# Kernel tuning notes

Hardware: AMD Instinct MI355X
Metric: run time of the kernel (lower is better)

The kernel has to match this reference:

```python
import jax, jax.numpy as jnp
import numpy as np

DIM, NHEADS = 1536, 12
HEAD_DIM = DIM // NHEADS  # 128

def _rope_params(max_pos, d):
    inv = 1.0 / (10000.0 ** (np.arange(0, d, 2, dtype=np.float64) / d))
    ang = np.outer(np.arange(max_pos, dtype=np.float64), inv)
    return np.stack([np.cos(ang), np.sin(ang)], -1).astype(np.float32)  # [max_pos, d//2, 2]

def setup_inputs() -> dict:
    key = jax.random.key(0)
    ks = jax.random.split(key, 8)
    B, F, H, W = 1, 3, 30, 52
    L = F * H * W  # 4680
    def w(k):
        return jax.random.normal(k, (DIM, DIM), jnp.float32) * 0.02
    # Wan rope table: head_dim=128 -> segments of real dim 44, 42, 42 (complex 22,21,21)
    freqs = np.concatenate([_rope_params(1024, 44), _rope_params(1024, 42), _rope_params(1024, 42)], axis=1)
    return {
        "x": jax.random.normal(ks[0], (B, L, DIM), jnp.float32),
        "wq": w(ks[1]), "bq": jnp.zeros((DIM,), jnp.float32),
        "wk": w(ks[2]), "bk": jnp.zeros((DIM,), jnp.float32),
        "wv": w(ks[3]), "bv": jnp.zeros((DIM,), jnp.float32),
        "wo": w(ks[4]), "bo": jnp.zeros((DIM,), jnp.float32),
        "gq": jnp.ones((DIM,), jnp.float32),
        "gk": jnp.ones((DIM,), jnp.float32),
        "freqs": jnp.asarray(freqs),                       # [1024, 64, 2] (cos, sin)
        "seq_lens": jnp.array([L], jnp.int64),
        "grid_sizes": jnp.array([[F, H, W]], jnp.int64),
        "F": F, "H": H, "W": W,
        "sink_size": 1, "local_attn_size": 2,
    }

def _rmsnorm(x, g, eps=1e-6):
    xf = x.astype(jnp.float32)
    return xf * jax.lax.rsqrt(jnp.mean(xf * xf, -1, keepdims=True) + eps) * g

def _rope_table(freqs, F, H, W):
    # freqs: [1024, 64, 2]; split complex dims [22, 21, 21] for (t, h, w)
    c = freqs.shape[1]
    s0 = c - 2 * (c // 3)          # 22
    s1 = c // 3                    # 21
    ft = jnp.broadcast_to(freqs[:F, :s0].reshape(F, 1, 1, s0, 2), (F, H, W, s0, 2))
    fh = jnp.broadcast_to(freqs[:H, s0:s0 + s1].reshape(1, H, 1, s1, 2), (F, H, W, s1, 2))
    fw = jnp.broadcast_to(freqs[:W, s0 + s1:].reshape(1, 1, W, s1, 2), (F, H, W, s1, 2))
    return jnp.concatenate([ft, fh, fw], -2).reshape(F * H * W, c, 2)  # [L, c, 2]

def _apply_rope(t, fr):
    # t: [B, L, n, d]; fr: [L, c, 2] with c = d // 2; complex multiply in real arithmetic
    B, L, n, d = t.shape
    c = d // 2
    tr = t.reshape(B, L, n, c, 2)
    a, b = tr[..., 0], tr[..., 1]
    cos = fr[None, :, None, :, 0]
    sin = fr[None, :, None, :, 1]
    out = jnp.stack([a * cos - b * sin, a * sin + b * cos], -1)
    return out.reshape(B, L, n, d)

def reference(x, wq, bq, wk, bk, wv, bv, wo, bo, gq, gk, freqs, seq_lens, grid_sizes,
              F, H, W, sink_size, local_attn_size):
    B, L, dim = x.shape
    n, d = NHEADS, HEAD_DIM
    q = _rmsnorm(x @ wq.T + bq, gq).reshape(B, L, n, d)
    k = _rmsnorm(x @ wk.T + bk, gk).reshape(B, L, n, d)
    v = (x @ wv.T + bv).reshape(B, L, n, d)
    fr = _rope_table(freqs, F, H, W)
    rq = _apply_rope(q, fr)
    rk = _apply_rope(k, fr)
    # sink + causal local-window block mask at frame granularity
    frame = jnp.arange(L) // (H * W)
    fq, fk = frame[:, None], frame[None, :]
    allow = (fk <= fq) & ((fk < sink_size) | (fq - fk < local_attn_size))  # [L, L]
    scores = jnp.einsum('blnd,bmnd->bnlm', rq, rk) / jnp.sqrt(jnp.float32(d))
    scores = jnp.where(allow[None, None], scores, -jnp.inf)
    p = jax.nn.softmax(scores, axis=-1)
    out = jnp.einsum('bnlm,bmnd->blnd', p, v).reshape(B, L, dim)
    return out @ wo.T + bo
```

## Files before the change

### kernel.cpp

```cpp
#include <hip/hip_runtime.h>

#define L_SEQ 4680
#define DIMSZ 1536
#define NHEAD 12
#define HDIM 128
#define FRAME 1560
#define NKT_ALL 74
#define SCALE_L2E 0.12751743f
#define WSZ 2359296
#define XSZ 7274496
#define PMPITCH 4736

typedef float f32x4 __attribute__((ext_vector_type(4)));
typedef _Float16 f16;
typedef _Float16 f16x2 __attribute__((ext_vector_type(2)));
typedef _Float16 f16x4 __attribute__((ext_vector_type(4)));
typedef _Float16 f16x8 __attribute__((ext_vector_type(8)));
typedef unsigned short u16;

__device__ __forceinline__ void gll16(const void* g, void* l) {
  __builtin_amdgcn_global_load_lds(
      (const __attribute__((address_space(1))) unsigned int*)g,
      (__attribute__((address_space(3))) unsigned int*)l, 16, 0, 0);
}

__global__ __launch_bounds__(256) void split_a16(
    const float* __restrict__ A, int R, f16* __restrict__ out) {
  const int rt = blockIdx.x, kt = blockIdx.y;
  const int t = threadIdx.x;
  const int row = t >> 1, c0 = (t & 1) * 16;
  const int gr = min(rt * 128 + row, R - 1);
  const float* src = &A[(size_t)gr * DIMSZ + kt * 32 + c0];
  float f[16];
#pragma unroll
  for (int i = 0; i < 4; ++i) *(float4*)&f[i * 4] = *(const float4*)&src[i * 4];
  size_t obase = ((size_t)(rt * 48 + kt)) * 4096 + row * 32;
#pragma unroll
  for (int cc = 0; cc < 2; ++cc) {
    f16x8 o;
#pragma unroll
    for (int i = 0; i < 8; ++i) o[i] = (f16)f[cc * 8 + i];
    int s = (c0 >> 3) + cc;
    *(f16x8*)&out[obase + ((s * 8) ^ ((row & 3) * 8))] = o;
  }
}

__global__ __launch_bounds__(256) void split_w16x3(
    const float* __restrict__ s0, const float* __restrict__ s1, const float* __restrict__ s2,
    f16* __restrict__ hi_base, f16* __restrict__ lo_base) {
  const int z = blockIdx.z;
  const float* A = z == 0 ? s0 : (z == 1 ? s1 : s2);
  f16* hi = hi_base + (size_t)z * WSZ;
  f16* lo8 = lo_base + (size_t)z * WSZ;
  const int rt = blockIdx.x, kt = blockIdx.y;
  const int t = threadIdx.x;
  const int row = t >> 1, c0 = (t & 1) * 16;
  const float* src = &A[(size_t)(rt * 128 + row) * DIMSZ + kt * 32 + c0];
  float f[16];
#pragma unroll
  for (int i = 0; i < 4; ++i) *(float4*)&f[i * 4] = *(const float4*)&src[i * 4];
  size_t obase = ((size_t)(rt * 48 + kt)) * 4096 + row * 32;
#pragma unroll
  for (int cc = 0; cc < 2; ++cc) {
    f16x8 oh, ol;
#pragma unroll
    for (int i = 0; i < 8; ++i) {
      float v = f[cc * 8 + i];
      f16 h = (f16)v;
      oh[i] = h;
      ol[i] = (f16)((v - (float)h) * 256.0f);
    }
    int s = (c0 >> 3) + cc;
    size_t off = obase + ((s * 8) ^ ((row & 3) * 8));
    *(f16x8*)&hi[off] = oh;
    *(f16x8*)&lo8[off] = ol;
  }
}

__global__ __launch_bounds__(256) void split_w16(
    const float* __restrict__ A, f16* __restrict__ hi, f16* __restrict__ lo8) {
  const int rt = blockIdx.x, kt = blockIdx.y;
  const int t = threadIdx.x;
  const int row = t >> 1, c0 = (t & 1) * 16;
  const float* src = &A[(size_t)(rt * 128 + row) * DIMSZ + kt * 32 + c0];
  float f[16];
#pragma unroll
  for (int i = 0; i < 4; ++i) *(float4*)&f[i * 4] = *(const float4*)&src[i * 4];
  size_t obase = ((size_t)(rt * 48 + kt)) * 4096 + row * 32;
#pragma unroll
  for (int cc = 0; cc < 2; ++cc) {
    f16x8 oh, ol;
#pragma unroll
    for (int i = 0; i < 8; ++i) {
      float v = f[cc * 8 + i];
      f16 h = (f16)v;
      oh[i] = h;
      ol[i] = (f16)((v - (float)h) * 256.0f);
    }
    int s = (c0 >> 3) + cc;
    size_t off = obase + ((s * 8) ^ ((row & 3) * 8));
    *(f16x8*)&hi[off] = oh;
    *(f16x8*)&lo8[off] = ol;
  }
}

__global__ __launch_bounds__(256, 3) void gemm_f16(
    const f16* __restrict__ A, const f16* __restrict__ Wh, const f16* __restrict__ Wl,
    const float* __restrict__ b0, const float* __restrict__ b1, const float* __restrict__ b2,
    float* __restrict__ C, int M) {
  __shared__ f16 S[2][3][4096];
  const int t = threadIdx.x;
  const int lane = t & 63, w = t >> 6;
  const int g = lane >> 4, ln = lane & 15;
  const int wm = w >> 1, wn = w & 1;
  const int mt = blockIdx.x, nt = blockIdx.y;
  const int which = nt / 12, ntw = nt - which * 12;
  const float* bias = which == 0 ? b0 : (which == 1 ? b1 : b2);
  const f16* srcs[3] = {A + (size_t)mt * 48 * 4096,
                        Wh + ((size_t)which * 12 + ntw) * 48 * 4096,
                        Wl + ((size_t)which * 12 + ntw) * 48 * 4096};
  float* Cw = C + (size_t)which * ((size_t)L_SEQ * DIMSZ);
  f32x4 acc[4][4] = {};
#pragma unroll
  for (int a = 0; a < 3; ++a)
#pragma unroll
    for (int i = 0; i < 2; ++i)
      gll16(srcs[a] + (i * 256 + t) * 8, &S[0][a][(i * 256 + t) * 8]);
  int buf = 0;
  const f16 sc = (f16)0.00390625f;
  for (int kt = 0; kt < 48; ++kt) {
    __syncthreads();
    if (kt + 1 < 48) {
      int b = buf ^ 1;
#pragma unroll
      for (int a = 0; a < 3; ++a)
#pragma unroll
        for (int i = 0; i < 2; ++i)
          gll16(srcs[a] + (size_t)(kt + 1) * 4096 + (i * 256 + t) * 8,
                &S[b][a][(i * 256 + t) * 8]);
    }
    f16x8 af[4], as[4], wh4[4], wl4[4];
#pragma unroll
    for (int mi = 0; mi < 4; ++mi) {
      int row = wm * 64 + mi * 16 + ln;
      int off = row * 32 + ((g * 8) ^ ((row & 3) * 8));
      af[mi] = *(const f16x8*)&S[buf][0][off];
#pragma unroll
      for (int i = 0; i < 8; ++i) as[mi][i] = af[mi][i] * sc;
    }
#pragma unroll
    for (int ni = 0; ni < 4; ++ni) {
      int row = wn * 64 + ni * 16 + ln;
      int off = row * 32 + ((g * 8) ^ ((row & 3) * 8));
      wh4[ni] = *(const f16x8*)&S[buf][1][off];
      wl4[ni] = *(const f16x8*)&S[buf][2][off];
    }
#pragma unroll
    for (int mi = 0; mi < 4; ++mi)
#pragma unroll
      for (int ni = 0; ni < 4; ++ni) {
        acc[mi][ni] = __builtin_amdgcn_mfma_f32_16x16x32_f16(af[mi], wh4[ni], acc[mi][ni], 0, 0, 0);
        acc[mi][ni] = __builtin_amdgcn_mfma_f32_16x16x32_f16(as[mi], wl4[ni], acc[mi][ni], 0, 0, 0);
      }
    buf ^= 1;
  }
#pragma unroll
  for (int mi = 0; mi < 4; ++mi)
#pragma unroll
    for (int ni = 0; ni < 4; ++ni) {
      int col = ntw * 128 + wn * 64 + ni * 16 + ln;
      float bv = bias[col];
#pragma unroll
      for (int r = 0; r < 4; ++r) {
        int row = mt * 128 + wm * 64 + mi * 16 + 4 * g + r;
        if (row < M) Cw[(size_t)row * DIMSZ + col] = acc[mi][ni][r] + bv;
      }
    }
}

__global__ __launch_bounds__(256) void norm_rope(
    const float* __restrict__ qf, const float* __restrict__ kf,
    const float* __restrict__ gq, const float* __restrict__ gk,
    const float* __restrict__ freqs, f16* __restrict__ q16, f16* __restrict__ k16) {
  const int pos = blockIdx.x;
  const bool isq = blockIdx.y == 0;
  const float* row = (isq ? qf : kf) + (size_t)pos * DIMSZ;
  const float* g = isq ? gq : gk;
  const int t = threadIdx.x;
  float2 ab[3];
  float ss = 0.f;
#pragma unroll
  for (int i = 0; i < 3; ++i) {
    ab[i] = *(const float2*)&row[2 * (t + 256 * i)];
    ss += ab[i].x * ab[i].x + ab[i].y * ab[i].y;
  }
#pragma unroll
  for (int m = 32; m; m >>= 1) ss += __shfl_xor(ss, m);
  __shared__ float part[4];
  if ((t & 63) == 0) part[t >> 6] = ss;
  __syncthreads();
  const float tot = part[0] + part[1] + part[2] + part[3];
  float scale = rsqrtf(tot * (1.f / DIMSZ) + 1e-6f);
  if (isq) scale *= SCALE_L2E;
  const int f = pos / FRAME;
  const int rem = pos - f * FRAME;
  const int hh = rem / 52;
  const int ww = rem - hh * 52;
  const int kt = pos >> 6, kk = pos & 63;
#pragma unroll
  for (int i = 0; i < 3; ++i) {
    const int p = t + 256 * i;
    const int c = p & 63;
    const int h = p >> 6;
    const int pr = c < 22 ? f : (c < 43 ? hh : ww);
    const float cs = freqs[(pr * 64 + c) * 2 + 0];
    const float sn = freqs[(pr * 64 + c) * 2 + 1];
    const float a = ab[i].x * scale * g[2 * p];
    const float b = ab[i].y * scale * g[2 * p + 1];
    f16x2 o;
    o[0] = (f16)(a * cs - b * sn);
    o[1] = (f16)(a * sn + b * cs);
    if (isq) {
      *(f16x2*)&q16[(size_t)pos * DIMSZ + 2 * p] = o;
    } else {
      const int s = c >> 2;
      size_t base = ((size_t)(h * NKT_ALL + kt)) << 13;
      *(f16x2*)&k16[base + kk * 128 + ((s * 8) ^ ((kk & 7) * 8)) + (c & 3) * 2] = o;
    }
  }
}

__global__ __launch_bounds__(256) void vconvert(const float* __restrict__ v, f16* __restrict__ v16) {
  __shared__ f16 Ls[64][136];
  const int kt = blockIdx.x, h = blockIdx.y, t = threadIdx.x;
#pragma unroll
  for (int p = 0; p < 8; ++p) {
    int e = p * 1024 + t * 4;
    int kk = e >> 7, d = e & 127;
    int gr = kt * 64 + kk;
    float4 val = make_float4(0.f, 0.f, 0.f, 0.f);
    if (gr < L_SEQ) val = *(const float4*)&v[(size_t)gr * DIMSZ + h * HDIM + d];
    f16x4 o;
    o[0] = (f16)val.x; o[1] = (f16)val.y; o[2] = (f16)val.z; o[3] = (f16)val.w;
    *(f16x4*)&Ls[kk][d] = o;
  }
  __syncthreads();
  f16* out = v16 + (((size_t)(h * NKT_ALL + kt)) << 13);
#pragma unroll
  for (int p = 0; p < 4; ++p) {
    int idx = p * 256 + t;
    int d = idx >> 3, c = idx & 7;
    const int nbb = (c & 1) * 2;
    const int g4 = (c >> 1) * 4;
    f16x8 o;
#pragma unroll
    for (int i = 0; i < 8; ++i) o[i] = Ls[(nbb + (i >> 2)) * 16 + g4 + (i & 3)][d];
    *(f16x8*)&out[d * 64 + 8 * (c ^ (d & 7))] = o;
  }
}

__global__ __launch_bounds__(256, 2) void attn_split(
    const f16* __restrict__ q16, const f16* __restrict__ k16,
    const f16* __restrict__ v16, float* __restrict__ pO,
    float* __restrict__ pm, float* __restrict__ pl) {
  __shared__ f16 Ks[2][8192];
  __shared__ f16 Vt[8192];
  __shared__ float Os[4][16][20];
  const int b = blockIdx.x;
  const int qt = 36 - b / 24;
  const int rem = b % 24;
  const int s = rem / 12;
  const int h = rem % 12;
  const int q0 = qt * 128;
  const int t = threadIdx.x;
  const int lane = t & 63, w = t >> 6;
  const int g = lane >> 4, ln = lane & 15;

  f16x8 qa[2][4];
  int klim[2];
  float m_run[2], l_run[2];
#pragma unroll
  for (int mi = 0; mi < 2; ++mi) {
    int qrow = min(q0 + w * 32 + mi * 16 + ln, L_SEQ - 1);
    klim[mi] = (qrow / FRAME + 1) * FRAME;
    m_run[mi] = -1e30f;
    l_run[mi] = 0.f;
    const f16* qb = &q16[(size_t)qrow * DIMSZ + h * HDIM + g * 8];
#pragma unroll
    for (int kc = 0; kc < 4; ++kc) qa[mi][kc] = *(const f16x8*)&qb[kc * 32];
  }
  const int klim0 = __shfl(klim[0], 0);
  f32x4 acc[2][8] = {};

  const int rmax = min(q0 + 127, L_SEQ - 1);
  const int nkt = ((rmax / FRAME + 1) * FRAME + 63) >> 6;
  const size_t hbase = ((size_t)h * NKT_ALL) << 13;

  f16x8 vv0, vv1, vv2, vv3;
  {
    const f16* tv = v16 + hbase + ((size_t)s << 13) + t * 8;
    vv0 = *(const f16x8*)(tv);
    vv1 = *(const f16x8*)(tv + 2048);
    vv2 = *(const f16x8*)(tv + 4096);
    vv3 = *(const f16x8*)(tv + 6144);
    f16* lv = Vt + t * 8;
    *(f16x8*)(lv) = vv0;
    *(f16x8*)(lv + 2048) = vv1;
    *(f16x8*)(lv + 4096) = vv2;
    *(f16x8*)(lv + 6144) = vv3;
    const f16* tk = k16 + hbase + ((size_t)s << 13);
#pragma unroll
    for (int i = 0; i < 4; ++i) gll16(tk + (i * 256 + t) * 8, &Ks[0][(i * 256 + t) * 8]);
  }
  int cur = 0;
  for (int kt = s; kt < nkt; kt += 2) {
    __syncthreads();
    const bool more = (kt + 2 < nkt);
    if (more) {
      size_t tb = hbase + ((size_t)(kt + 2) << 13);
      const f16* tk = k16 + tb;
#pragma unroll
      for (int i = 0; i < 4; ++i) gll16(tk + (i * 256 + t) * 8, &Ks[cur ^ 1][(i * 256 + t) * 8]);
      const f16* tv = v16 + tb + t * 8;
      vv0 = *(const f16x8*)(tv);
      vv1 = *(const f16x8*)(tv + 2048);
      vv2 = *(const f16x8*)(tv + 4096);
      vv3 = *(const f16x8*)(tv + 6144);
    }
    const f16* Kb = Ks[cur];

    f32x4 st[2][4] = {};
    __builtin_amdgcn_s_setprio(1);
#pragma unroll
    for (int nb = 0; nb < 4; ++nb) {
      int row = nb * 16 + ln;
#pragma unroll
      for (int kc = 0; kc < 4; ++kc) {
        f16x8 kb = *(const f16x8*)&Kb[row * 128 + ((g * 8 + kc * 32) ^ ((row & 7) * 8))];
        st[0][nb] = __builtin_amdgcn_mfma_f32_16x16x32_f16(kb, qa[0][kc], st[0][nb], 0, 0, 0);
        st[1][nb] = __builtin_amdgcn_mfma_f32_16x16x32_f16(kb, qa[1][kc], st[1][nb], 0, 0, 0);
      }
    }
    __builtin_amdgcn_s_setprio(0);

    f16x4 pb[2][4];
    const bool boundary = (kt * 64 + 64 > klim0);
#pragma unroll
    for (int mi = 0; mi < 2; ++mi) {
      float rm = -1e30f;
      if (boundary) {
#pragma unroll
        for (int nb = 0; nb < 4; ++nb)
#pragma unroll
          for (int r = 0; r < 4; ++r) {
            int key = kt * 64 + nb * 16 + 4 * g + r;
            float val = st[mi][nb][r];
            if (key >= klim[mi]) val = -1e30f;
            st[mi][nb][r] = val;
            rm = fmaxf(rm, val);
          }
      } else {
#pragma unroll
        for (int nb = 0; nb < 4; ++nb)
#pragma unroll
          for (int r = 0; r < 4; ++r) rm = fmaxf(rm, st[mi][nb][r]);
      }
      rm = fmaxf(rm, __shfl_xor(rm, 16));
      rm = fmaxf(rm, __shfl_xor(rm, 32));
      if (!__all(rm - m_run[mi] <= 8.0f)) {
        float mn = fmaxf(m_run[mi], rm);
        float fs = exp2f(m_run[mi] - mn);
        m_run[mi] = mn;
        l_run[mi] *= fs;
#pragma unroll
        for (int db = 0; db < 8; ++db)
#pragma unroll
          for (int r = 0; r < 4; ++r) acc[mi][db][r] *= fs;
      }
      float sm = 0.f;
#pragma unroll
      for (int nb = 0; nb < 4; ++nb)
#pragma unroll
        for (int r = 0; r < 4; ++r) {
          float e = exp2f(st[mi][nb][r] - m_run[mi]);
          sm += e;
          pb[mi][nb][r] = (f16)e;
        }
      sm += __shfl_xor(sm, 16);
      sm += __shfl_xor(sm, 32);
      l_run[mi] += sm;
    }

    __builtin_amdgcn_s_setprio(1);
#pragma unroll
    for (int db = 0; db < 8; ++db) {
      int d = db * 16 + ln;
#pragma unroll
      for (int nbp = 0; nbp < 2; ++nbp) {
        f16x8 vvv = *(const f16x8*)&Vt[d * 64 + 8 * ((g * 2 + nbp) ^ (d & 7))];
        f16x4 vlo = {vvv[0], vvv[1], vvv[2], vvv[3]};
        f16x4 vhi = {vvv[4], vvv[5], vvv[6], vvv[7]};
        acc[0][db] = __builtin_amdgcn_mfma_f32_16x16x16f16(vlo, pb[0][2 * nbp], acc[0][db], 0, 0, 0);
        acc[1][db] = __builtin_amdgcn_mfma_f32_16x16x16f16(vlo, pb[1][2 * nbp], acc[1][db], 0, 0, 0);
        acc[0][db] = __builtin_amdgcn_mfma_f32_16x16x16f16(vhi, pb[0][2 * nbp + 1], acc[0][db], 0, 0, 0);
        acc[1][db] = __builtin_amdgcn_mfma_f32_16x16x16f16(vhi, pb[1][2 * nbp + 1], acc[1][db], 0, 0, 0);
      }
    }
    __builtin_amdgcn_s_setprio(0);

    __syncthreads();
    if (more) {
      f16* lv = Vt + t * 8;
      *(f16x8*)(lv) = vv0;
      *(f16x8*)(lv + 2048) = vv1;
      *(f16x8*)(lv + 4096) = vv2;
      *(f16x8*)(lv + 6144) = vv3;
    }
    cur ^= 1;
  }

#pragma unroll
  for (int mi = 0; mi < 2; ++mi) {
    int qrow = q0 + w * 32 + mi * 16 + ln;
    if (g == 0) {
      pm[((size_t)s * 12 + h) * PMPITCH + qrow] = m_run[mi];
      pl[((size_t)s * 12 + h) * PMPITCH + qrow] = l_run[mi];
    }
#pragma unroll
    for (int db = 0; db < 8; ++db) {
      *(f32x4*)&Os[w][ln][4 * g] = acc[mi][db];
      asm volatile("s_waitcnt lgkmcnt(0)" ::: "memory");
#pragma unroll
      for (int r = 0; r < 4; ++r) {
        int q = q0 + w * 32 + mi * 16 + 4 * g + r;
        float val = Os[w][4 * g + r][ln];
        if (q < L_SEQ)
          pO[((size_t)s * L_SEQ + q) * DIMSZ + h * HDIM + db * 16 + ln] = val;
      }
      asm volatile("s_waitcnt lgkmcnt(0)" ::: "memory");
    }
  }
}

__global__ __launch_bounds__(256) void combine_k(
    const float* __restrict__ pO, const float* __restrict__ pm,
    const float* __restrict__ pl, f16* __restrict__ aos) {
  const int qt = blockIdx.x, h = blockIdx.y, t = threadIdx.x;
  const int row = t >> 1, d0 = (t & 1) * 64;
  const int q = min(qt * 128 + row, L_SEQ - 1);
  const float m0 = pm[(size_t)h * PMPITCH + q];
  const float m1 = pm[((size_t)12 + h) * PMPITCH + q];
  const float l0 = pl[(size_t)h * PMPITCH + q];
  const float l1 = pl[((size_t)12 + h) * PMPITCH + q];
  const float m = fmaxf(m0, m1);
  float w0 = exp2f(m0 - m), w1 = exp2f(m1 - m);
  const float rinv = 1.f / (w0 * l0 + w1 * l1);
  w0 *= rinv; w1 *= rinv;
  const float* o0 = &pO[(size_t)q * DIMSZ + h * HDIM + d0];
  const float* o1 = &pO[((size_t)L_SEQ + q) * DIMSZ + h * HDIM + d0];
  f16* outbase = aos + ((size_t)qt * 48 + h * 4) * 4096 + row * 32;
#pragma unroll
  for (int c8 = 0; c8 < 8; ++c8) {
    float a[8], bvals[8];
    *(float4*)&a[0] = *(const float4*)&o0[c8 * 8];
    *(float4*)&a[4] = *(const float4*)&o0[c8 * 8 + 4];
    *(float4*)&bvals[0] = *(const float4*)&o1[c8 * 8];
    *(float4*)&bvals[4] = *(const float4*)&o1[c8 * 8 + 4];
    f16x8 ov;
#pragma unroll
    for (int i = 0; i < 8; ++i) ov[i] = (f16)(w0 * a[i] + w1 * bvals[i]);
    int d = d0 + c8 * 8;
    int ktb = d >> 5;
    int s8 = (d & 31) >> 3;
    *(f16x8*)&outbase[(size_t)ktb * 4096 + ((s8 * 8) ^ ((row & 3) * 8))] = ov;
  }
}

extern "C" void kernel_launch(void* const* d_in, const int* in_sizes, int n_in,
                              void* d_out, int out_size, void* d_ws, size_t ws_size,
                              hipStream_t stream) {
  const float* x  = (const float*)d_in[0];
  const float* wq = (const float*)d_in[1];
  const float* bq = (const float*)d_in[2];
  const float* wk = (const float*)d_in[3];
  const float* bk = (const float*)d_in[4];
  const float* wv = (const float*)d_in[5];
  const float* bv = (const float*)d_in[6];
  const float* wo = (const float*)d_in[7];
  const float* bo = (const float*)d_in[8];
  const float* gq = (const float*)d_in[9];
  const float* gk = (const float*)d_in[10];
  const float* freqs = (const float*)d_in[11];
  float* out = (float*)d_out;
  float* ws = (float*)d_ws;

  const size_t LD = (size_t)L_SEQ * DIMSZ;

  float* qf = ws;
  float* kf = ws + LD;
  float* vf = ws + 2 * LD;
  f16* xs  = (f16*)(ws + 3 * LD);
  f16* k16 = xs + XSZ;
  f16* v16 = k16 + XSZ;
  f16* whi = v16 + XSZ;
  f16* wlo = whi + 3 * (size_t)WSZ;
  f16* q16 = xs;
  float* pO = qf;
  f16* aos = (f16*)vf;
  float* pm = vf + XSZ / 2;
  float* pl = pm + 2 * 12 * PMPITCH;
  f16* wo_hi = (f16*)(pl + 2 * 12 * PMPITCH);
  f16* wo_lo = wo_hi + (size_t)WSZ;

  dim3 blk(256);
  split_a16<<<dim3(37, 48), blk, 0, stream>>>(x, L_SEQ, xs);
  split_w16x3<<<dim3(12, 48, 3), blk, 0, stream>>>(wq, wk, wv, whi, wlo);
  gemm_f16<<<dim3(37, 36), blk, 0, stream>>>(xs, whi, wlo, bq, bk, bv, qf, L_SEQ);
  norm_rope<<<dim3(L_SEQ, 2), blk, 0, stream>>>(qf, kf, gq, gk, freqs, q16, k16);
  vconvert<<<dim3(NKT_ALL, NHEAD), blk, 0, stream>>>(vf, v16);
  split_w16<<<dim3(12, 48), blk, 0, stream>>>(wo, wo_hi, wo_lo);
  attn_split<<<dim3(37 * 24), blk, 0, stream>>>(q16, k16, v16, pO, pm, pl);
  combine_k<<<dim3(37, 12), blk, 0, stream>>>(pO, pm, pl, aos);
  gemm_f16<<<dim3(37, 12), blk, 0, stream>>>(aos, wo_hi, wo_lo, bo, bo, bo, out, L_SEQ);
}
```

Baseline: 450.3 us.

## Drop fp16 lo-split weight correction and merge all conversion kernels

```diff
diff --git a/kernel.cpp b/kernel.cpp
--- a/kernel.cpp
+++ b/kernel.cpp
@@ -24,91 +24,45 @@
       (__attribute__((address_space(3))) unsigned int*)l, 16, 0, 0);
 }
 
-__global__ __launch_bounds__(256) void split_a16(
-    const float* __restrict__ A, int R, f16* __restrict__ out) {
-  const int rt = blockIdx.x, kt = blockIdx.y;
+__global__ __launch_bounds__(256) void split_all(
+    const float* __restrict__ x,  const float* __restrict__ wq,
+    const float* __restrict__ wk, const float* __restrict__ wv,
+    const float* __restrict__ wo, f16* __restrict__ xs,
+    f16* __restrict__ whi) {
+  const int kt = blockIdx.x;
+  const int y = blockIdx.y;
+  const float* src; f16* dst; int R, rt;
+  if (y < 37) { src = x; dst = xs; R = L_SEQ; rt = y; }
+  else {
+    int i = y - 37;
+    int z = i / 12; rt = i - z * 12; R = DIMSZ;
+    src = z == 0 ? wq : (z == 1 ? wk : (z == 2 ? wv : wo));
+    dst = whi + (size_t)z * WSZ;
+  }
   const int t = threadIdx.x;
   const int row = t >> 1, c0 = (t & 1) * 16;
   const int gr = min(rt * 128 + row, R - 1);
-  const float* src = &A[(size_t)gr * DIMSZ + kt * 32 + c0];
+  const float* s = &src[(size_t)gr * DIMSZ + kt * 32 + c0];
   float f[16];
 #pragma unroll
-  for (int i = 0; i < 4; ++i) *(float4*)&f[i * 4] = *(const float4*)&src[i * 4];
+  for (int i = 0; i < 4; ++i) *(float4*)&f[i * 4] = *(const float4*)&s[i * 4];
   size_t obase = ((size_t)(rt * 48 + kt)) * 4096 + row * 32;
 #pragma unroll
   for (int cc = 0; cc < 2; ++cc) {
     f16x8 o;
 #pragma unroll
     for (int i = 0; i < 8; ++i) o[i] = (f16)f[cc * 8 + i];
-    int s = (c0 >> 3) + cc;
-    *(f16x8*)&out[obase + ((s * 8) ^ ((row & 3) * 8))] = o;
-  }
-}
-
-__global__ __launch_bounds__(256) void split_w16x3(
-    const float* __restrict__ s0, const float* __restrict__ s1, const float* __restrict__ s2,
-    f16* __restrict__ hi_base, f16* __restrict__ lo_base) {
-  const int z = blockIdx.z;
-  const float* A = z == 0 ? s0 : (z == 1 ? s1 : s2);
-  f16* hi = hi_base + (size_t)z * WSZ;
-  f16* lo8 = lo_base + (size_t)z * WSZ;
-  const int rt = blockIdx.x, kt = blockIdx.y;
-  const int t = threadIdx.x;
-  const int row = t >> 1, c0 = (t & 1) * 16;
-  const float* src = &A[(size_t)(rt * 128 + row) * DIMSZ + kt * 32 + c0];
-  float f[16];
-#pragma unroll
-  for (int i = 0; i < 4; ++i) *(float4*)&f[i * 4] = *(const float4*)&src[i * 4];
-  size_t obase = ((size_t)(rt * 48 + kt)) * 4096 + row * 32;
-#pragma unroll
-  for (int cc = 0; cc < 2; ++cc) {
-    f16x8 oh, ol;
-#pragma unroll
-    for (int i = 0; i < 8; ++i) {
-      float v = f[cc * 8 + i];
-      f16 h = (f16)v;
-      oh[i] = h;
-      ol[i] = (f16)((v - (float)h) * 256.0f);
-    }
-    int s = (c0 >> 3) + cc;
-    size_t off = obase + ((s * 8) ^ ((row & 3) * 8));
-    *(f16x8*)&hi[off] = oh;
-    *(f16x8*)&lo8[off] = ol;
-  }
-}
-
-__global__ __launch_bounds__(256) void split_w16(
-    const float* __restrict__ A, f16* __restrict__ hi, f16* __restrict__ lo8) {
-  const int rt = blockIdx.x, kt = blockIdx.y;
-  const int t = threadIdx.x;
-  const int row = t >> 1, c0 = (t & 1) * 16;
-  const float* src = &A[(size_t)(rt * 128 + row) * DIMSZ + kt * 32 + c0];
-  float f[16];
-#pragma unroll
-  for (int i = 0; i < 4; ++i) *(float4*)&f[i * 4] = *(const float4*)&src[i * 4];
-  size_t obase = ((size_t)(rt * 48 + kt)) * 4096 + row * 32;
-#pragma unroll
-  for (int cc = 0; cc < 2; ++cc) {
-    f16x8 oh, ol;
-#pragma unroll
-    for (int i = 0; i < 8; ++i) {
-      float v = f[cc * 8 + i];
-      f16 h = (f16)v;
-      oh[i] = h;
-      ol[i] = (f16)((v - (float)h) * 256.0f);
-    }
-    int s = (c0 >> 3) + cc;
-    size_t off = obase + ((s * 8) ^ ((row & 3) * 8));
-    *(f16x8*)&hi[off] = oh;
-    *(f16x8*)&lo8[off] = ol;
-  }
-}
-
-__global__ __launch_bounds__(256, 3) void gemm_f16(
-    const f16* __restrict__ A, const f16* __restrict__ Wh, const f16* __restrict__ Wl,
+    int sl = (c0 >> 3) + cc;
+    *(f16x8*)&dst[obase + ((sl * 8) ^ ((row & 3) * 8))] = o;
+  }
+}
+
+__global__ __launch_bounds__(256, 3) void gemm_f16_1p(
+    const f16* __restrict__ A, const f16* __restrict__ Wh,
     const float* __restrict__ b0, const float* __restrict__ b1, const float* __restrict__ b2,
     float* __restrict__ C, int M) {
-  __shared__ f16 S[2][3][4096];
+  __shared__ f16 SA[8192];
+  __shared__ f16 SW[8192];
   const int t = threadIdx.x;
   const int lane = t & 63, w = t >> 6;
   const int g = lane >> 4, ln = lane & 15;
@@ -116,53 +70,40 @@
   const int mt = blockIdx.x, nt = blockIdx.y;
   const int which = nt / 12, ntw = nt - which * 12;
   const float* bias = which == 0 ? b0 : (which == 1 ? b1 : b2);
-  const f16* srcs[3] = {A + (size_t)mt * 48 * 4096,
-                        Wh + ((size_t)which * 12 + ntw) * 48 * 4096,
-                        Wl + ((size_t)which * 12 + ntw) * 48 * 4096};
+  const f16* srcA = A + (size_t)mt * 48 * 4096;
+  const f16* srcW = Wh + ((size_t)which * 12 + ntw) * 48 * 4096;
   float* Cw = C + (size_t)which * ((size_t)L_SEQ * DIMSZ);
   f32x4 acc[4][4] = {};
-#pragma unroll
-  for (int a = 0; a < 3; ++a)
-#pragma unroll
-    for (int i = 0; i < 2; ++i)
-      gll16(srcs[a] + (i * 256 + t) * 8, &S[0][a][(i * 256 + t) * 8]);
-  int buf = 0;
-  const f16 sc = (f16)0.00390625f;
-  for (int kt = 0; kt < 48; ++kt) {
+  for (int kt2 = 0; kt2 < 24; ++kt2) {
     __syncthreads();
-    if (kt + 1 < 48) {
-      int b = buf ^ 1;
-#pragma unroll
-      for (int a = 0; a < 3; ++a)
-#pragma unroll
-        for (int i = 0; i < 2; ++i)
-          gll16(srcs[a] + (size_t)(kt + 1) * 4096 + (i * 256 + t) * 8,
-                &S[b][a][(i * 256 + t) * 8]);
-    }
-    f16x8 af[4], as[4], wh4[4], wl4[4];
-#pragma unroll
-    for (int mi = 0; mi < 4; ++mi) {
-      int row = wm * 64 + mi * 16 + ln;
-      int off = row * 32 + ((g * 8) ^ ((row & 3) * 8));
-      af[mi] = *(const f16x8*)&S[buf][0][off];
-#pragma unroll
-      for (int i = 0; i < 8; ++i) as[mi][i] = af[mi][i] * sc;
-    }
-#pragma unroll
-    for (int ni = 0; ni < 4; ++ni) {
-      int row = wn * 64 + ni * 16 + ln;
-      int off = row * 32 + ((g * 8) ^ ((row & 3) * 8));
-      wh4[ni] = *(const f16x8*)&S[buf][1][off];
-      wl4[ni] = *(const f16x8*)&S[buf][2][off];
-    }
-#pragma unroll
-    for (int mi = 0; mi < 4; ++mi)
+    size_t ko = (size_t)kt2 * 8192;
+#pragma unroll
+    for (int i = 0; i < 4; ++i) {
+      gll16(srcA + ko + (i * 256 + t) * 8, &SA[(i * 256 + t) * 8]);
+      gll16(srcW + ko + (i * 256 + t) * 8, &SW[(i * 256 + t) * 8]);
+    }
+    __syncthreads();
+#pragma unroll
+    for (int kc = 0; kc < 2; ++kc) {
+      f16x8 af[4], wh4[4];
+#pragma unroll
+      for (int mi = 0; mi < 4; ++mi) {
+        int row = wm * 64 + mi * 16 + ln;
+        af[mi] = *(const f16x8*)&SA[kc * 4096 + row * 32 + ((g * 8) ^ ((row & 3) * 8))];
+      }
 #pragma unroll
       for (int ni = 0; ni < 4; ++ni) {
-        acc[mi][ni] = __builtin_amdgcn_mfma_f32_16x16x32_f16(af[mi], wh4[ni], acc[mi][ni], 0, 0, 0);
-        acc[mi][ni] = __builtin_amdgcn_mfma_f32_16x16x32_f16(as[mi], wl4[ni], acc[mi][ni], 0, 0, 0);
-      }
-    buf ^= 1;
+        int row = wn * 64 + ni * 16 + ln;
+        wh4[ni] = *(const f16x8*)&SW[kc * 4096 + row * 32 + ((g * 8) ^ ((row & 3) * 8))];
+      }
+      __builtin_amdgcn_s_setprio(1);
+#pragma unroll
+      for (int mi = 0; mi < 4; ++mi)
+#pragma unroll
+        for (int ni = 0; ni < 4; ++ni)
+          acc[mi][ni] = __builtin_amdgcn_mfma_f32_16x16x32_f16(af[mi], wh4[ni], acc[mi][ni], 0, 0, 0);
+      __builtin_amdgcn_s_setprio(0);
+    }
   }
 #pragma unroll
   for (int mi = 0; mi < 4; ++mi)
@@ -503,23 +444,19 @@
   f16* k16 = xs + XSZ;
   f16* v16 = k16 + XSZ;
   f16* whi = v16 + XSZ;
-  f16* wlo = whi + 3 * (size_t)WSZ;
   f16* q16 = xs;
   float* pO = qf;
   f16* aos = (f16*)vf;
   float* pm = vf + XSZ / 2;
   float* pl = pm + 2 * 12 * PMPITCH;
-  f16* wo_hi = (f16*)(pl + 2 * 12 * PMPITCH);
-  f16* wo_lo = wo_hi + (size_t)WSZ;
+  f16* wo_hi = whi + 3 * (size_t)WSZ;
 
   dim3 blk(256);
-  split_a16<<<dim3(37, 48), blk, 0, stream>>>(x, L_SEQ, xs);
-  split_w16x3<<<dim3(12, 48, 3), blk, 0, stream>>>(wq, wk, wv, whi, wlo);
-  gemm_f16<<<dim3(37, 36), blk, 0, stream>>>(xs, whi, wlo, bq, bk, bv, qf, L_SEQ);
+  split_all<<<dim3(48, 85), blk, 0, stream>>>(x, wq, wk, wv, wo, xs, whi);
+  gemm_f16_1p<<<dim3(37, 36), blk, 0, stream>>>(xs, whi, bq, bk, bv, qf, L_SEQ);
   norm_rope<<<dim3(L_SEQ, 2), blk, 0, stream>>>(qf, kf, gq, gk, freqs, q16, k16);
   vconvert<<<dim3(NKT_ALL, NHEAD), blk, 0, stream>>>(vf, v16);
-  split_w16<<<dim3(12, 48), blk, 0, stream>>>(wo, wo_hi, wo_lo);
   attn_split<<<dim3(37 * 24), blk, 0, stream>>>(q16, k16, v16, pO, pm, pl);
   combine_k<<<dim3(37, 12), blk, 0, stream>>>(pO, pm, pl, aos);
-  gemm_f16<<<dim3(37, 12), blk, 0, stream>>>(aos, wo_hi, wo_lo, bo, bo, bo, out, L_SEQ);
-}
+  gemm_f16_1p<<<dim3(37, 12), blk, 0, stream>>>(aos, wo_hi, bo, bo, bo, out, L_SEQ);
+}
```

Result: faster. 385.1 us (-14.5%).
